# Optimization experiments

Hardware: AMD Instinct MI355X
Metric: run time of the kernel (lower is better)

## Reference

```python
import jax, jax.numpy as jnp
import numpy as np

DIM = 512
NUM_HEADS = 8
HEAD_DIM = DIM // NUM_HEADS
LOCAL_HEADS = 4
WINDOW = 64
NEG_INF = -1e9


def setup_inputs() -> dict:
    key = jax.random.key(0)
    ks = jax.random.split(key, 5)
    B, N, C = 4, 8192, DIM
    x = jax.random.normal(ks[0], (B, N, C), dtype=jnp.float32)
    # nn.Linear weights stored as [out, in]; xavier-ish scale
    s = (2.0 / (C + C)) ** 0.5
    Wq = jax.random.normal(ks[1], (C, C), dtype=jnp.float32) * s
    Wkv = jax.random.normal(ks[2], (C, C), dtype=jnp.float32) * s
    Wproj = jax.random.normal(ks[3], (C, C), dtype=jnp.float32) * s
    bproj = jax.random.normal(ks[4], (C,), dtype=jnp.float32) * 0.01
    return {"x": x, "Wq": Wq, "Wkv": Wkv, "Wproj": Wproj, "bproj": bproj}


def _look_around(t):
    # t: [B,H,nw,m,d] -> [B,H,nw,3m,d] (prev window, current, next; zero-padded at ends)
    p = jnp.pad(t, ((0, 0), (0, 0), (1, 1), (0, 0), (0, 0)))
    return jnp.concatenate([p[:, :, :-2], p[:, :, 1:-1], p[:, :, 2:]], axis=3)


def _local_attn(q, k, v, m):
    # non-causal LocalAttention, look_backward=1, look_forward=1
    B, H, N, d = q.shape
    nw = N // m
    scale = d ** -0.5
    qw = q.reshape(B, H, nw, m, d)
    kw = _look_around(k.reshape(B, H, nw, m, d))
    vw = _look_around(v.reshape(B, H, nw, m, d))
    # mask out look-around positions that fall outside the sequence
    pos = jnp.arange(N).reshape(nw, m)
    pp = jnp.pad(pos, ((1, 1), (0, 0)), constant_values=-1)
    kpos = jnp.concatenate([pp[:-2], pp[1:-1], pp[2:]], axis=1)  # [nw, 3m]
    valid = (kpos >= 0)[None, None, :, None, :]
    scores = jnp.einsum('bhwid,bhwjd->bhwij', qw * scale, kw)
    scores = jnp.where(valid, scores, NEG_INF)
    attn = jax.nn.softmax(scores, axis=-1)
    out = jnp.einsum('bhwij,bhwjd->bhwid', attn, vw)
    return out.reshape(B, H, N, d)


def _linear_attn(q, k, v):
    d = q.shape[-1]
    q = jax.nn.softmax(q, axis=-1) * (d ** -0.5)
    k = jax.nn.softmax(k, axis=-2)
    context = jnp.einsum('bhnd,bhne->bhde', k, v)
    return jnp.einsum('bhnd,bhde->bhne', q, context)


def reference(x, Wq, Wkv, Wproj, bproj):
    B, N, C = x.shape
    m = WINDOW
    original_N = N
    rem = N % m  # static; 0 for chosen shapes
    if rem > 0:
        x = jnp.pad(x, ((0, 0), (m - rem, 0), (0, 0)))
        N = x.shape[1]
    q = x @ Wq.T
    k = x @ Wkv.T
    v = x @ Wkv.T  # source uses the same kv linear for both k and v
    merge = lambda t: t.reshape(B, N, -1, HEAD_DIM).transpose(0, 2, 1, 3)  # [B,H,N,d]
    q, k, v = merge(q), merge(k), merge(v)
    lh = LOCAL_HEADS
    lq, gq = q[:, :lh], q[:, lh:]
    lk, gk = k[:, :lh], k[:, lh:]
    lv, gv = v[:, :lh], v[:, lh:]
    outs = []
    if lh > 0:
        outs.append(_local_attn(lq, lk, lv, m))
    if q.shape[1] - lh > 0:
        outs.append(_linear_attn(gq, gk, gv))
    attn = jnp.concatenate(outs, axis=1)  # [B,H,N,d]
    y = attn.transpose(0, 2, 1, 3).reshape(B, N, -1)
    y = y[:, -original_N:]
    y = y @ Wproj.T + bproj
    return (y, attn)
```

## Files before the change

kernel.cpp:

```cpp
#include <hip/hip_runtime.h>

#define DIM 512
#define NH 8
#define HD 64
#define LH 4
#define WIN 64
#define BATCH 4
#define SEQ 8192
#define NWIN (SEQ/WIN)

typedef unsigned short u16;
typedef __bf16 bf16x8 __attribute__((ext_vector_type(8)));
typedef float f32x4 __attribute__((ext_vector_type(4)));

__device__ __forceinline__ float b2f(u16 u) {
    return __uint_as_float(((unsigned int)u) << 16);
}
__device__ __forceinline__ u16 f2b(float f) {
    unsigned int x = __float_as_uint(f);
    return (u16)((x + 0x7FFFu + ((x >> 16) & 1u)) >> 16);
}

__device__ __forceinline__ void gload16(const void* g, void* l) {
    __builtin_amdgcn_global_load_lds(
        (__attribute__((address_space(1))) void*)g,
        (__attribute__((address_space(3))) void*)l, 16, 0, 0);
}

__global__ void convert_bf16(const float* __restrict__ src, u16* __restrict__ dst, long n)
{
    long i = ((long)blockIdx.x * 256 + threadIdx.x) * 8;
    const long stride = (long)gridDim.x * 256 * 8;
    for (; i < n; i += stride) {
        uint4 a = *(const uint4*)(src + i), b = *(const uint4*)(src + i + 4);
        const float* af = (const float*)&a;
        const float* bf_ = (const float*)&b;
        uint4 o; u16* ou = (u16*)&o;
        #pragma unroll
        for (int j = 0; j < 4; j++) { ou[j] = f2b(af[j]); ou[4 + j] = f2b(bf_[j]); }
        *(uint4*)(dst + i) = o;
    }
}

__global__ void convert_w3(const float* __restrict__ Wq, const float* __restrict__ Wkv,
                           const float* __restrict__ Wp, u16* __restrict__ Wqk,
                           u16* __restrict__ Wproj_b)
{
    const int slice = blockIdx.y;
    const float* src = (slice == 0) ? Wq : (slice == 1) ? Wkv : Wp;
    u16* dst = (slice == 0) ? Wqk : (slice == 1) ? (Wqk + DIM * DIM) : Wproj_b;
    long i = ((long)blockIdx.x * 256 + threadIdx.x) * 8;
    if (i >= (long)DIM * DIM) return;
    uint4 a = *(const uint4*)(src + i), b = *(const uint4*)(src + i + 4);
    const float* af = (const float*)&a;
    const float* bf_ = (const float*)&b;
    uint4 o; u16* ou = (u16*)&o;
    #pragma unroll
    for (int j = 0; j < 4; j++) { ou[j] = f2b(af[j]); ou[4 + j] = f2b(bf_[j]); }
    *(uint4*)(dst + i) = o;
}

__global__ __launch_bounds__(256) void gemm_qk_tiled(const u16* __restrict__ xb,
        const u16* __restrict__ Wqk, u16* __restrict__ qh, u16* __restrict__ kh,
        u16* __restrict__ khTg)
{
    __shared__ __align__(16) u16 smem[16384];
    u16* lA = smem;
    u16* lB = smem + 8192;

    const int tid = threadIdx.x;
    const int wv = tid >> 6, lane = tid & 63;
    const int quad = lane >> 4, l16 = lane & 15;
    const int wr = wv >> 1, wc = wv & 1;
    const int row0 = blockIdx.y * 128;
    const int col0 = blockIdx.x * 128;
    const int srow = lane >> 3;
    const int scol = ((lane & 7) ^ srow) * 8;

    f32x4 acc[4][4];
    #pragma unroll
    for (int t = 0; t < 4; t++)
        for (int u = 0; u < 4; u++)
            for (int i = 0; i < 4; i++) acc[t][u][i] = 0.f;

    const u16* gA = xb  + (size_t)(row0 + srow) * DIM + scol;
    const u16* gB = Wqk + (size_t)(col0 + srow) * DIM + scol;

    for (int kt = 0; kt < DIM; kt += 64) {
        __syncthreads();
        #pragma unroll
        for (int i = 0; i < 4; i++) {
            int rb = wv * 32 + i * 8;
            gload16(gA + (size_t)rb * DIM + kt, &lA[rb * 64]);
            gload16(gB + (size_t)rb * DIM + kt, &lB[rb * 64]);
        }
        __syncthreads();
        #pragma unroll
        for (int kc = 0; kc < 2; kc++) {
            bf16x8 af[4], bfr[4];
            #pragma unroll
            for (int t = 0; t < 4; t++) {
                int row = wr * 64 + t * 16 + l16;
                int slot = (kc * 4 + quad) ^ (row & 7);
                af[t] = *(const bf16x8*)&lA[row * 64 + slot * 8];
            }
            #pragma unroll
            for (int u = 0; u < 4; u++) {
                int row = wc * 64 + u * 16 + l16;
                int slot = (kc * 4 + quad) ^ (row & 7);
                bfr[u] = *(const bf16x8*)&lB[row * 64 + slot * 8];
            }
            #pragma unroll
            for (int t = 0; t < 4; t++)
                #pragma unroll
                for (int u = 0; u < 4; u++)
                    acc[t][u] = __builtin_amdgcn_mfma_f32_16x16x32_bf16(af[t], bfr[u], acc[t][u], 0, 0, 0);
        }
    }

    __syncthreads();
    u16* cw = smem + wv * 4096;
    #pragma unroll
    for (int t = 0; t < 4; t++)
        #pragma unroll
        for (int u = 0; u < 4; u++)
            #pragma unroll
            for (int r = 0; r < 4; r++)
                cw[(t * 16 + quad * 4 + r) * 64 + u * 16 + l16] = f2b(acc[t][u][r]);

    const int colg0 = col0 + wc * 64;
    const int seg = lane & 7;
    u16* dstbase;
    {
        int h = (colg0 & 511) >> 6;
        u16* base = (colg0 < 512) ? qh : kh;
        dstbase = base + (size_t)h * SEQ * HD;
    }
    #pragma unroll
    for (int i = 0; i < 8; i++) {
        int mm = i * 8 + (lane >> 3);
        uint4 v = *(const uint4*)&cw[mm * 64 + seg * 8];
        int m = row0 + wr * 64 + mm;
        int bb = m >> 13, nn = m & (SEQ - 1);
        *(uint4*)(dstbase + ((size_t)bb * NH * SEQ + nn) * HD + seg * 8) = v;
    }

    if (colg0 >= 768) {
        int hg = ((colg0 & 511) >> 6) - 4;
        int m0 = row0 + wr * 64;
        int bb = m0 >> 13, nn0 = m0 & (SEQ - 1);
        u16* kT = khTg + ((size_t)((bb << 2) + hg) * 64) * SEQ + nn0;
        #pragma unroll
        for (int i = 0; i < 8; i++) {
            int e = i * 8 + (lane >> 3);
            int ns = (lane & 7) * 8;
            uint4 ov; u16* op = (u16*)&ov;
            #pragma unroll
            for (int j = 0; j < 8; j++) op[j] = cw[(ns + j) * 64 + e];
            *(uint4*)(kT + (size_t)e * SEQ + ns) = ov;
        }
    }
}

#define KJ_STRIDE 72
#define KT_STRIDE 200
#define OT_STRIDE 80

__global__ __launch_bounds__(256) void local_attn(const u16* __restrict__ qh,
        const u16* __restrict__ kh, float* __restrict__ attn_out,
        u16* __restrict__ attn_b)
{
    __shared__ __align__(16) u16 kjP[192 * KJ_STRIDE];
    __shared__ __align__(16) u16 kT[64 * KT_STRIDE];

    const int w = blockIdx.x;
    const int bh = blockIdx.y;
    const int b = bh >> 2, h = bh & 3;
    const int tid = threadIdx.x;
    const int wv = tid >> 6, lane = tid & 63;
    const int quad = lane >> 4, l16 = lane & 15;

    for (int idx = tid; idx < 192 * 8; idx += 256) {
        int j = idx >> 3, dc = (idx & 7) << 3;
        int n = w * WIN - WIN + j;
        uint4 val = make_uint4(0, 0, 0, 0);
        if (n >= 0 && n < SEQ)
            val = *(const uint4*)(kh + (((size_t)(b * NH + h)) * SEQ + n) * HD + dc);
        *(uint4*)(&kjP[j * KJ_STRIDE + dc]) = val;
    }
    __syncthreads();
    for (int idx = tid; idx < 64 * 192; idx += 256) {
        int e = idx & 63, j = idx >> 6;
        kT[e * KT_STRIDE + j] = kjP[j * KJ_STRIDE + e];
    }
    __syncthreads();

    f32x4 s[12];
    #pragma unroll
    for (int t = 0; t < 12; t++)
        for (int i = 0; i < 4; i++) s[t][i] = 0.f;

    const u16* qrow = qh + (((size_t)(b * NH + h)) * SEQ + w * WIN + wv * 16 + l16) * HD + quad * 8;
    #pragma unroll
    for (int kk = 0; kk < 64; kk += 32) {
        bf16x8 a = *(const bf16x8*)(qrow + kk);
        #pragma unroll
        for (int t = 0; t < 12; t++) {
            bf16x8 bf = *(const bf16x8*)(&kjP[(t * 16 + l16) * KJ_STRIDE + kk + quad * 8]);
            s[t] = __builtin_amdgcn_mfma_f32_16x16x32_bf16(a, bf, s[t], 0, 0, 0);
        }
    }
    __syncthreads();

    const float scale = 0.125f;
    #pragma unroll
    for (int r = 0; r < 4; r++) {
        float vals[12];
        float mx = -3.0e38f;
        #pragma unroll
        for (int t = 0; t < 12; t++) {
            int j = t * 16 + l16;
            float v = s[t][r] * scale;
            bool valid = !((w == 0 && j < 64) || (w == NWIN - 1 && j >= 128));
            v = valid ? v : -30000.0f;
            vals[t] = v;
            mx = fmaxf(mx, v);
        }
        for (int m = 1; m <= 8; m <<= 1) mx = fmaxf(mx, __shfl_xor(mx, m));
        float sum = 0.f;
        #pragma unroll
        for (int t = 0; t < 12; t++) { vals[t] = __expf(vals[t] - mx); sum += vals[t]; }
        for (int m = 1; m <= 8; m <<= 1) sum += __shfl_xor(sum, m);
        float inv = 1.0f / sum;
        int prow = wv * 16 + quad * 4 + r;
        #pragma unroll
        for (int t = 0; t < 12; t++)
            kjP[prow * KT_STRIDE + t * 16 + l16] = f2b(vals[t] * inv);
    }
    __syncthreads();

    f32x4 o[4];
    #pragma unroll
    for (int t = 0; t < 4; t++)
        for (int i = 0; i < 4; i++) o[t][i] = 0.f;
    #pragma unroll
    for (int kc = 0; kc < 6; kc++) {
        bf16x8 a = *(const bf16x8*)(&kjP[(wv * 16 + l16) * KT_STRIDE + kc * 32 + quad * 8]);
        #pragma unroll
        for (int t = 0; t < 4; t++) {
            bf16x8 bf = *(const bf16x8*)(&kT[(t * 16 + l16) * KT_STRIDE + kc * 32 + quad * 8]);
            o[t] = __builtin_amdgcn_mfma_f32_16x16x32_bf16(a, bf, o[t], 0, 0, 0);
        }
    }
    #pragma unroll
    for (int t = 0; t < 4; t++) {
        int e = t * 16 + l16;
        #pragma unroll
        for (int r = 0; r < 4; r++) {
            int n = w * WIN + wv * 16 + quad * 4 + r;
            attn_out[(((size_t)(b * NH + h)) * SEQ + n) * HD + e] = o[t][r];
        }
    }
    __syncthreads();
    #pragma unroll
    for (int t = 0; t < 4; t++)
        #pragma unroll
        for (int r = 0; r < 4; r++)
            kT[(wv * 16 + quad * 4 + r) * OT_STRIDE + t * 16 + l16] = f2b(o[t][r]);
    __syncthreads();
    for (int idx = tid; idx < 512; idx += 256) {
        int row = idx >> 3, seg = (idx & 7) * 8;
        uint4 v = *(const uint4*)&kT[row * OT_STRIDE + seg];
        *(uint4*)(attn_b + ((size_t)(b * SEQ + w * WIN + row)) * DIM + h * HD + seg) = v;
    }
}

__global__ __launch_bounds__(256) void ctx_accum(const u16* __restrict__ khTg,
        float* __restrict__ partials, float* __restrict__ colsum)
{
    const int chunk = blockIdx.x;
    const int bh = blockIdx.y;
    const int tid = threadIdx.x;
    const int wv = tid >> 6, lane = tid & 63;
    const int quad = lane >> 4, l16 = lane & 15;

    __shared__ __align__(16) u16 rawL[64 * 64];
    __shared__ __align__(16) u16 expL[64 * 64];

    const u16* base = khTg + (size_t)bh * 64 * SEQ;
    const int dexp = tid >> 2;
    const int nsub = (tid & 3) * 16;

    const int srow = lane >> 3;
    const int scol = ((lane & 7) ^ srow) * 8;

    f32x4 acc[4];
    #pragma unroll
    for (int u = 0; u < 4; u++)
        for (int i = 0; i < 4; i++) acc[u][i] = 0.f;
    float csum = 0.f;

    for (int t = 0; t < 4; t++) {
        const int n0 = chunk * 256 + t * 64;
        __syncthreads();
        #pragma unroll
        for (int i = 0; i < 2; i++) {
            int r0 = wv * 16 + i * 8;
            gload16(base + (size_t)(r0 + srow) * SEQ + n0 + scol, &rawL[r0 * 64]);
        }
        {
            const u16* g = base + (size_t)dexp * SEQ + n0 + nsub;
            uint4 v0 = *(const uint4*)g;
            uint4 v1 = *(const uint4*)(g + 8);
            const u16* ua = (const u16*)&v0;
            const u16* ub = (const u16*)&v1;
            uint4 o0, o1; u16* pa = (u16*)&o0; u16* pb = (u16*)&o1;
            #pragma unroll
            for (int j = 0; j < 8; j++) {
                u16 ra = f2b(__expf(b2f(ua[j])));
                u16 rb = f2b(__expf(b2f(ub[j])));
                pa[j] = ra; pb[j] = rb;
                csum += b2f(ra) + b2f(rb);
            }
            int sl0 = ((nsub >> 3) + 0) ^ (dexp & 7);
            int sl1 = ((nsub >> 3) + 1) ^ (dexp & 7);
            *(uint4*)&expL[dexp * 64 + sl0 * 8] = o0;
            *(uint4*)&expL[dexp * 64 + sl1 * 8] = o1;
        }
        __syncthreads();
        #pragma unroll
        for (int kc = 0; kc < 2; kc++) {
            int arow = wv * 16 + l16;
            bf16x8 af = *(const bf16x8*)&expL[arow * 64 + (((kc * 4 + quad) ^ (arow & 7)) * 8)];
            #pragma unroll
            for (int u = 0; u < 4; u++) {
                int brow = u * 16 + l16;
                bf16x8 bf = *(const bf16x8*)&rawL[brow * 64 + (((kc * 4 + quad) ^ (brow & 7)) * 8)];
                acc[u] = __builtin_amdgcn_mfma_f32_16x16x32_bf16(af, bf, acc[u], 0, 0, 0);
            }
        }
    }

    float* P = partials + ((size_t)(chunk * 16 + bh)) * 4096;
    #pragma unroll
    for (int u = 0; u < 4; u++)
        #pragma unroll
        for (int r = 0; r < 4; r++)
            P[(wv * 16 + quad * 4 + r) * 64 + u * 16 + l16] = acc[u][r];

    csum += __shfl_xor(csum, 1);
    csum += __shfl_xor(csum, 2);
    if ((tid & 3) == 0) atomicAdd(colsum + bh * 64 + dexp, csum);
}

__global__ __launch_bounds__(256) void reduce_ctx(const float* __restrict__ partials,
        const float* __restrict__ colsum, u16* __restrict__ ctxT)
{
    const int quarter = blockIdx.x;
    const int bh = blockIdx.y;
    const int tid = threadIdx.x;
    __shared__ float cs[64];
    if (tid < 64) cs[tid] = colsum[bh * 64 + tid];
    __syncthreads();
    const int i0 = quarter * 1024;
    for (int idx = i0 + tid; idx < i0 + 1024; idx += 256) {
        float s = 0.f;
        #pragma unroll 8
        for (int c = 0; c < 32; c++)
            s += partials[((size_t)(c * 16 + bh)) * 4096 + idx];
        int d = idx >> 6, e = idx & 63;
        ctxT[(size_t)bh * 4096 + e * 64 + d] = f2b(s / cs[d]);
    }
}

__global__ __launch_bounds__(256) void global_out(const u16* __restrict__ qh,
        const u16* __restrict__ ctxT, float* __restrict__ attn_out,
        u16* __restrict__ attn_b)
{
    const int nblk = blockIdx.x;
    const int bh = blockIdx.y;
    const int b = bh >> 2, hg = bh & 3;
    const int tid = threadIdx.x;
    const int wv = tid >> 6, lane = tid & 63;
    const int quad = lane >> 4, l16 = lane & 15;

    __shared__ __align__(16) u16 ctxL[64 * 64];
    __shared__ __align__(16) u16 ot[64 * OT_STRIDE];

    {
        const int srow = lane >> 3;
        const int scol = ((lane & 7) ^ srow) * 8;
        const u16* src = ctxT + (size_t)bh * 4096 + (size_t)srow * 64 + scol;
        #pragma unroll
        for (int j = 0; j < 2; j++) {
            int rb = j * 32 + wv * 8;
            gload16(src + rb * 64, &ctxL[rb * 64]);
        }
    }

    const int n0 = nblk * 64;
    const u16* qp = qh + (((size_t)(b * NH + LH + hg)) * SEQ + n0 + wv * 16 + l16) * HD + quad * 8;
    uint4 v0 = *(const uint4*)(qp);
    uint4 v1 = *(const uint4*)(qp + 32);
    const u16* u0 = (const u16*)&v0;
    const u16* u1 = (const u16*)&v1;
    float e0[8], e1[8];
    float s = 0.f;
    #pragma unroll
    for (int j = 0; j < 8; j++) { e0[j] = __expf(b2f(u0[j])); s += e0[j]; }
    #pragma unroll
    for (int j = 0; j < 8; j++) { e1[j] = __expf(b2f(u1[j])); s += e1[j]; }
    s += __shfl_xor(s, 16);
    s += __shfl_xor(s, 32);
    const float inv = 0.125f / s;
    uint4 p0u, p1u;
    u16* p0 = (u16*)&p0u; u16* p1 = (u16*)&p1u;
    #pragma unroll
    for (int j = 0; j < 8; j++) { p0[j] = f2b(e0[j] * inv); p1[j] = f2b(e1[j] * inv); }
    bf16x8 pa0 = *(const bf16x8*)&p0u;
    bf16x8 pa1 = *(const bf16x8*)&p1u;

    __syncthreads();

    f32x4 acc[4];
    #pragma unroll
    for (int u = 0; u < 4; u++)
        for (int i = 0; i < 4; i++) acc[u][i] = 0.f;
    #pragma unroll
    for (int u = 0; u < 4; u++) {
        int row = u * 16 + l16;
        int s0 = (0 + quad) ^ (row & 7);
        int s1 = (4 + quad) ^ (row & 7);
        bf16x8 b0 = *(const bf16x8*)&ctxL[row * 64 + s0 * 8];
        bf16x8 b1 = *(const bf16x8*)&ctxL[row * 64 + s1 * 8];
        acc[u] = __builtin_amdgcn_mfma_f32_16x16x32_bf16(pa0, b0, acc[u], 0, 0, 0);
        acc[u] = __builtin_amdgcn_mfma_f32_16x16x32_bf16(pa1, b1, acc[u], 0, 0, 0);
    }

    const size_t obase = ((size_t)(b * NH + LH + hg)) * SEQ + n0 + wv * 16;
    #pragma unroll
    for (int u = 0; u < 4; u++) {
        int ee = u * 16 + l16;
        #pragma unroll
        for (int r = 0; r < 4; r++)
            attn_out[(obase + quad * 4 + r) * HD + ee] = acc[u][r];
    }

    #pragma unroll
    for (int u = 0; u < 4; u++)
        #pragma unroll
        for (int r = 0; r < 4; r++)
            ot[(wv * 16 + quad * 4 + r) * OT_STRIDE + u * 16 + l16] = f2b(acc[u][r]);
    __syncthreads();
    for (int idx = tid; idx < 512; idx += 256) {
        int row = idx >> 3, seg = (idx & 7) * 8;
        uint4 vv = *(const uint4*)&ot[row * OT_STRIDE + seg];
        *(uint4*)(attn_b + ((size_t)(b * SEQ + n0 + row)) * DIM + (LH + hg) * HD + seg) = vv;
    }
}

__global__ __launch_bounds__(256) void proj_gemm_tiled(const u16* __restrict__ attn_b,
        const u16* __restrict__ Wproj, const float* __restrict__ bproj,
        float* __restrict__ y)
{
    __shared__ __align__(16) u16 smem[16384];
    u16* lA = smem;
    u16* lB = smem + 8192;

    const int tid = threadIdx.x;
    const int wv = tid >> 6, lane = tid & 63;
    const int quad = lane >> 4, l16 = lane & 15;
    const int wr = wv >> 1, wc = wv & 1;
    const int row0 = blockIdx.y * 128;
    const int col0 = blockIdx.x * 128;
    const int srow = lane >> 3;
    const int scol = ((lane & 7) ^ srow) * 8;

    f32x4 acc[4][4];
    #pragma unroll
    for (int t = 0; t < 4; t++)
        for (int u = 0; u < 4; u++)
            for (int i = 0; i < 4; i++) acc[t][u][i] = 0.f;

    const u16* gA = attn_b + (size_t)(row0 + srow) * DIM + scol;
    const u16* gB = Wproj  + (size_t)(col0 + srow) * DIM + scol;

    for (int kt = 0; kt < DIM; kt += 64) {
        __syncthreads();
        #pragma unroll
        for (int i = 0; i < 4; i++) {
            int rb = wv * 32 + i * 8;
            gload16(gA + (size_t)rb * DIM + kt, &lA[rb * 64]);
            gload16(gB + (size_t)rb * DIM + kt, &lB[rb * 64]);
        }
        __syncthreads();
        #pragma unroll
        for (int kc = 0; kc < 2; kc++) {
            bf16x8 af[4], bfr[4];
            #pragma unroll
            for (int t = 0; t < 4; t++) {
                int row = wr * 64 + t * 16 + l16;
                int slot = (kc * 4 + quad) ^ (row & 7);
                af[t] = *(const bf16x8*)&lA[row * 64 + slot * 8];
            }
            #pragma unroll
            for (int u = 0; u < 4; u++) {
                int row = wc * 64 + u * 16 + l16;
                int slot = (kc * 4 + quad) ^ (row & 7);
                bfr[u] = *(const bf16x8*)&lB[row * 64 + slot * 8];
            }
            #pragma unroll
            for (int t = 0; t < 4; t++)
                #pragma unroll
                for (int u = 0; u < 4; u++)
                    acc[t][u] = __builtin_amdgcn_mfma_f32_16x16x32_bf16(af[t], bfr[u], acc[t][u], 0, 0, 0);
        }
    }

    #pragma unroll
    for (int u = 0; u < 4; u++) {
        int col = col0 + wc * 64 + u * 16 + l16;
        float bias = bproj[col];
        #pragma unroll
        for (int t = 0; t < 4; t++)
            #pragma unroll
            for (int r = 0; r < 4; r++) {
                int m = row0 + wr * 64 + t * 16 + quad * 4 + r;
                y[(size_t)m * DIM + col] = acc[t][u][r] + bias;
            }
    }
}

extern "C" void kernel_launch(void* const* d_in, const int* in_sizes, int n_in,
                              void* d_out, int out_size, void* d_ws, size_t ws_size,
                              hipStream_t stream)
{
    (void)in_sizes; (void)n_in; (void)out_size; (void)ws_size;
    const float* x     = (const float*)d_in[0];
    const float* Wq    = (const float*)d_in[1];
    const float* Wkv   = (const float*)d_in[2];
    const float* Wproj = (const float*)d_in[3];
    const float* bproj = (const float*)d_in[4];

    float* y        = (float*)d_out;
    float* attn_out = y + (size_t)BATCH * SEQ * DIM;

    u16* xb = (u16*)y;
    u16* qh = xb + (size_t)BATCH * SEQ * DIM;

    float* partials = attn_out + (size_t)LH * SEQ * HD;

    char* ws = (char*)d_ws;
    u16*   ctxT    = (u16*)ws;
    float* colsum  = (float*)(ws + 262144);
    u16*   Wqk     = (u16*)(ws + 266240);
    u16*   Wproj_b = (u16*)(ws + 266240 + 1048576);
    u16*   kh      = (u16*)(ws + 266240 + 1048576 + 524288);
    u16*   attn_b  = kh + (size_t)BATCH * SEQ * DIM;
    u16*   khTg    = attn_b + (size_t)BATCH * SEQ * DIM;

    const long NX = (long)BATCH * SEQ * DIM;

    hipMemsetAsync(colsum, 0, 4096, stream);
    convert_bf16<<<4096, 256, 0, stream>>>(x, xb, NX);
    convert_w3<<<dim3(128, 3), 256, 0, stream>>>(Wq, Wkv, Wproj, Wqk, Wproj_b);

    gemm_qk_tiled<<<dim3(8, 256), 256, 0, stream>>>(xb, Wqk, qh, kh, khTg);
    local_attn<<<dim3(NWIN, 16), 256, 0, stream>>>(qh, kh, attn_out, attn_b);
    ctx_accum<<<dim3(32, 16), 256, 0, stream>>>(khTg, partials, colsum);
    reduce_ctx<<<dim3(4, 16), 256, 0, stream>>>(partials, colsum, ctxT);
    global_out<<<dim3(SEQ / 64, 16), 256, 0, stream>>>(qh, ctxT, attn_out, attn_b);
    proj_gemm_tiled<<<dim3(4, 256), 256, 0, stream>>>(attn_b, Wproj_b, bproj, y);
}
```

Baseline: 341.1 us.

## Emit transposed K for all heads from QK GEMM and load it in local attention

The QK GEMM epilogue now writes a transposed K layout for all eight heads instead of only the global heads. It skips the row-major K write for the global heads, and pads the epilogue LDS stride to 72 to reduce bank conflicts. Local attention now loads K-transposed tiles straight from global memory instead of transposing them element by element in shared memory, and ctx_accum indexes into the new layout. This trades extra global writes for local-head K-transpose against removing a slow scalar LDS transpose in local_attn.

```diff
diff --git a/kernel.cpp b/kernel.cpp
--- a/kernel.cpp
+++ b/kernel.cpp
@@ -62,9 +62,9 @@
 
 __global__ __launch_bounds__(256) void gemm_qk_tiled(const u16* __restrict__ xb,
         const u16* __restrict__ Wqk, u16* __restrict__ qh, u16* __restrict__ kh,
-        u16* __restrict__ khTg)
-{
-    __shared__ __align__(16) u16 smem[16384];
+        u16* __restrict__ khT)
+{
+    __shared__ __align__(16) u16 smem[18432];
     u16* lA = smem;
     u16* lB = smem + 8192;
 
@@ -119,44 +119,40 @@
     }
 
     __syncthreads();
-    u16* cw = smem + wv * 4096;
+    u16* cw = smem + wv * 4608;
     #pragma unroll
     for (int t = 0; t < 4; t++)
         #pragma unroll
         for (int u = 0; u < 4; u++)
             #pragma unroll
             for (int r = 0; r < 4; r++)
-                cw[(t * 16 + quad * 4 + r) * 64 + u * 16 + l16] = f2b(acc[t][u][r]);
+                cw[(t * 16 + quad * 4 + r) * 72 + u * 16 + l16] = f2b(acc[t][u][r]);
 
     const int colg0 = col0 + wc * 64;
+    const int h = (colg0 & 511) >> 6;
+    const bool is_q = colg0 < 512;
     const int seg = lane & 7;
-    u16* dstbase;
-    {
-        int h = (colg0 & 511) >> 6;
-        u16* base = (colg0 < 512) ? qh : kh;
-        dstbase = base + (size_t)h * SEQ * HD;
-    }
-    #pragma unroll
-    for (int i = 0; i < 8; i++) {
-        int mm = i * 8 + (lane >> 3);
-        uint4 v = *(const uint4*)&cw[mm * 64 + seg * 8];
-        int m = row0 + wr * 64 + mm;
-        int bb = m >> 13, nn = m & (SEQ - 1);
-        *(uint4*)(dstbase + ((size_t)bb * NH * SEQ + nn) * HD + seg * 8) = v;
-    }
-
-    if (colg0 >= 768) {
-        int hg = ((colg0 & 511) >> 6) - 4;
-        int m0 = row0 + wr * 64;
-        int bb = m0 >> 13, nn0 = m0 & (SEQ - 1);
-        u16* kT = khTg + ((size_t)((bb << 2) + hg) * 64) * SEQ + nn0;
+    const int m0 = row0 + wr * 64;
+    const int bb = m0 >> 13, nn0 = m0 & (SEQ - 1);
+
+    if (is_q || h < LH) {
+        u16* dstbase = (is_q ? qh : kh) + (size_t)h * SEQ * HD;
+        #pragma unroll
+        for (int i = 0; i < 8; i++) {
+            int mm = i * 8 + (lane >> 3);
+            uint4 v = *(const uint4*)&cw[mm * 72 + seg * 8];
+            *(uint4*)(dstbase + ((size_t)bb * NH * SEQ + nn0 + mm) * HD + seg * 8) = v;
+        }
+    }
+    if (!is_q) {
+        u16* kT = khT + (size_t)(bb * NH + h) * 64 * SEQ + nn0;
         #pragma unroll
         for (int i = 0; i < 8; i++) {
             int e = i * 8 + (lane >> 3);
-            int ns = (lane & 7) * 8;
+            int ns = seg * 8;
             uint4 ov; u16* op = (u16*)&ov;
             #pragma unroll
-            for (int j = 0; j < 8; j++) op[j] = cw[(ns + j) * 64 + e];
+            for (int j = 0; j < 8; j++) op[j] = cw[(ns + j) * 72 + e];
             *(uint4*)(kT + (size_t)e * SEQ + ns) = ov;
         }
     }
@@ -167,8 +163,8 @@
 #define OT_STRIDE 80
 
 __global__ __launch_bounds__(256) void local_attn(const u16* __restrict__ qh,
-        const u16* __restrict__ kh, float* __restrict__ attn_out,
-        u16* __restrict__ attn_b)
+        const u16* __restrict__ kh, const u16* __restrict__ khT,
+        float* __restrict__ attn_out, u16* __restrict__ attn_b)
 {
     __shared__ __align__(16) u16 kjP[192 * KJ_STRIDE];
     __shared__ __align__(16) u16 kT[64 * KT_STRIDE];
@@ -188,10 +184,16 @@
             val = *(const uint4*)(kh + (((size_t)(b * NH + h)) * SEQ + n) * HD + dc);
         *(uint4*)(&kjP[j * KJ_STRIDE + dc]) = val;
     }
-    __syncthreads();
-    for (int idx = tid; idx < 64 * 192; idx += 256) {
-        int e = idx & 63, j = idx >> 6;
-        kT[e * KT_STRIDE + j] = kjP[j * KJ_STRIDE + e];
+    {
+        const u16* kTbase = khT + (size_t)(b * NH + h) * 64 * SEQ;
+        for (int idx = tid; idx < 64 * 24; idx += 256) {
+            int e = idx / 24, jc = (idx - e * 24) * 8;
+            int n = w * WIN - WIN + jc;
+            uint4 val = make_uint4(0, 0, 0, 0);
+            if (n >= 0 && n <= SEQ - 8)
+                val = *(const uint4*)(kTbase + (size_t)e * SEQ + n);
+            *(uint4*)(&kT[e * KT_STRIDE + jc]) = val;
+        }
     }
     __syncthreads();
 
@@ -275,7 +277,7 @@
     }
 }
 
-__global__ __launch_bounds__(256) void ctx_accum(const u16* __restrict__ khTg,
+__global__ __launch_bounds__(256) void ctx_accum(const u16* __restrict__ khT,
         float* __restrict__ partials, float* __restrict__ colsum)
 {
     const int chunk = blockIdx.x;
@@ -287,7 +289,7 @@
     __shared__ __align__(16) u16 rawL[64 * 64];
     __shared__ __align__(16) u16 expL[64 * 64];
 
-    const u16* base = khTg + (size_t)bh * 64 * SEQ;
+    const u16* base = khT + (size_t)((bh >> 2) * NH + LH + (bh & 3)) * 64 * SEQ;
     const int dexp = tid >> 2;
     const int nsub = (tid & 3) * 16;
 
@@ -557,7 +559,7 @@
     u16*   Wproj_b = (u16*)(ws + 266240 + 1048576);
     u16*   kh      = (u16*)(ws + 266240 + 1048576 + 524288);
     u16*   attn_b  = kh + (size_t)BATCH * SEQ * DIM;
-    u16*   khTg    = attn_b + (size_t)BATCH * SEQ * DIM;
+    u16*   khT     = attn_b + (size_t)BATCH * SEQ * DIM;
 
     const long NX = (long)BATCH * SEQ * DIM;
 
@@ -565,9 +567,9 @@
     convert_bf16<<<4096, 256, 0, stream>>>(x, xb, NX);
     convert_w3<<<dim3(128, 3), 256, 0, stream>>>(Wq, Wkv, Wproj, Wqk, Wproj_b);
 
-    gemm_qk_tiled<<<dim3(8, 256), 256, 0, stream>>>(xb, Wqk, qh, kh, khTg);
-    local_attn<<<dim3(NWIN, 16), 256, 0, stream>>>(qh, kh, attn_out, attn_b);
-    ctx_accum<<<dim3(32, 16), 256, 0, stream>>>(khTg, partials, colsum);
+    gemm_qk_tiled<<<dim3(8, 256), 256, 0, stream>>>(xb, Wqk, qh, kh, khT);
+    local_attn<<<dim3(NWIN, 16), 256, 0, stream>>>(qh, kh, khT, attn_out, attn_b);
+    ctx_accum<<<dim3(32, 16), 256, 0, stream>>>(khT, partials, colsum);
     reduce_ctx<<<dim3(4, 16), 256, 0, stream>>>(partials, colsum, ctxT);
     global_out<<<dim3(SEQ / 64, 16), 256, 0, stream>>>(qh, ctxT, attn_out, attn_b);
     proj_gemm_tiled<<<dim3(4, 256), 256, 0, stream>>>(attn_b, Wproj_b, bproj, y);
```

New measurement: 347.1 us. No clear change (+1.8%).
